# Optimization experiments

Hardware: AMD Instinct MI355X
Metric: run time of the kernel (lower is better)

## Reference

```python
import jax, jax.numpy as jnp
import numpy as np

DIM = 1024
NUM_HEADS = 16
HEAD_DIM = DIM // NUM_HEADS
HIDDEN = 2 * DIM  # swiglu hidden


def rotate_half(x):
    x1, x2 = jnp.split(x, 2, axis=-1)
    return jnp.concatenate((-x2, x1), axis=-1)


def setup_inputs() -> dict:
    key = jax.random.key(0)
    ks = jax.random.split(key, 9)
    s = lambda fan_in: 1.0 / np.sqrt(fan_in)
    x = jax.random.normal(ks[0], (4, 2048, DIM), dtype=jnp.float32)
    qkv_w = jax.random.uniform(ks[1], (3 * DIM, DIM), minval=-s(DIM), maxval=s(DIM))
    proj_w = jax.random.uniform(ks[2], (DIM, DIM), minval=-s(DIM), maxval=s(DIM))
    proj_b = jax.random.uniform(ks[3], (DIM,), minval=-s(DIM), maxval=s(DIM))
    w1_w = jax.random.uniform(ks[4], (HIDDEN, DIM), minval=-s(DIM), maxval=s(DIM))
    w1_b = jnp.zeros((HIDDEN,), jnp.float32)
    w2_w = jax.random.uniform(ks[5], (HIDDEN, DIM), minval=-s(DIM), maxval=s(DIM))
    w2_b = jnp.zeros((HIDDEN,), jnp.float32)
    w3_w = jax.random.uniform(ks[6], (DIM, HIDDEN), minval=-s(HIDDEN), maxval=s(HIDDEN))
    w3_b = jnp.zeros((DIM,), jnp.float32)
    return {"x": x, "qkv_w": qkv_w, "proj_w": proj_w, "proj_b": proj_b,
            "w1_w": w1_w, "w1_b": w1_b, "w2_w": w2_w, "w2_b": w2_b,
            "w3_w": w3_w, "w3_b": w3_b}


def reference(x, qkv_w, proj_w, proj_b, w1_w, w1_b, w2_w, w2_b, w3_w, w3_b):
    B, N, C = x.shape
    H, D = NUM_HEADS, HEAD_DIM
    scale = D ** -0.5
    # QKV projection (no bias)
    qkv = jnp.einsum('bnc,fc->bnf', x, qkv_w).reshape(B, N, 3, H, D)
    qkv = jnp.transpose(qkv, (2, 0, 3, 1, 4))  # [3, B, H, N, D]
    q, k, v = qkv[0], qkv[1], qkv[2]
    # Rotary embeddings
    inv_freq = 1.0 / (10000.0 ** (jnp.arange(0, D, 2, dtype=jnp.float32) / D))
    t = jnp.arange(N, dtype=jnp.float32)
    freqs = jnp.einsum('i,j->ij', t, inv_freq)
    emb = jnp.concatenate((freqs, freqs), axis=-1)[None, None]  # [1,1,N,D]
    cos, sin = jnp.cos(emb), jnp.sin(emb)
    q = q * cos + rotate_half(q) * sin
    k = k * cos + rotate_half(k) * sin
    # Attention (non-causal, as in source)
    attn = jnp.einsum('bhnd,bhmd->bhnm', q, k) * scale
    attn = jax.nn.softmax(attn, axis=-1)
    out = jnp.einsum('bhnm,bhmd->bhnd', attn, v)
    out = jnp.transpose(out, (0, 2, 1, 3)).reshape(B, N, C)
    out = jnp.einsum('bnc,fc->bnf', out, proj_w) + proj_b
    # SwiGLU MLP
    x1 = jnp.einsum('bnc,fc->bnf', out, w1_w) + w1_b
    x2 = jnp.einsum('bnc,fc->bnf', out, w2_w) + w2_b
    hidden = jax.nn.silu(x1) * x2
    return jnp.einsum('bnh,fh->bnf', hidden, w3_w) + w3_b
```

## Files before the change

kernel.cpp:

```cpp
#include <hip/hip_runtime.h>
#include <hip/hip_bf16.h>
#include <math.h>


#define SEQ     2048
#define BATCH   4
#define NH      16
#define CDIM    1024
#define MROWS   8192

typedef __bf16 bf16x8 __attribute__((ext_vector_type(8)));
typedef float  floatx4 __attribute__((ext_vector_type(4)));
typedef float  floatx16 __attribute__((ext_vector_type(16)));
typedef unsigned int u32;

__device__ __forceinline__ unsigned short f2bf(float f) {
    __bf16 h = (__bf16)f;
    return __builtin_bit_cast(unsigned short, h);
}
__device__ __forceinline__ float fexp2(float x) {
    float r; asm("v_exp_f32 %0, %1" : "=v"(r) : "v"(x)); return r;
}
__device__ __forceinline__ floatx4 mfma16(bf16x8 a, bf16x8 b, floatx4 c) {
    return __builtin_amdgcn_mfma_f32_16x16x32_bf16(a, b, c, 0, 0, 0);
}
__device__ __forceinline__ floatx16 mfma32(bf16x8 a, bf16x8 b, floatx16 c) {
    return __builtin_amdgcn_mfma_f32_32x32x16_bf16(a, b, c, 0, 0, 0);
}
__device__ __forceinline__ void gld16(void* lds, const void* g) {
    __builtin_amdgcn_global_load_lds(
        (const __attribute__((address_space(1))) u32*)g,
        (__attribute__((address_space(3))) u32*)lds, 16, 0, 0);
}

template <int OUTMODE, bool BIAS>
__global__ __launch_bounds__(256) void mgemm(
    const unsigned short* __restrict__ A,
    const unsigned short* __restrict__ B,
    const float* __restrict__ bias,
    void* __restrict__ C, int ldc,
    int K)
{
    __shared__ __align__(16) unsigned short As[128 * 32];
    __shared__ __align__(16) unsigned short Bs[128 * 32];

    const int tid  = threadIdx.x;
    const int lane = tid & 63;
    const int wave = tid >> 6;
    const int l16  = lane & 15;
    const int quad = lane >> 4;
    const int wm = (wave >> 1) * 64, wn = (wave & 1) * 64;
    const int bm = blockIdx.y, bn = blockIdx.x;

    const unsigned short* Ag = A + (size_t)(bm * 128) * K;
    const unsigned short* Bg = B + (size_t)(bn * 128) * K;

    const int srow0 = wave * 32 + (lane >> 2);
    const int scol  = (lane & 3) * 8;
    unsigned short* lA0 = As + (wave * 2 + 0) * 512;
    unsigned short* lA1 = As + (wave * 2 + 1) * 512;
    unsigned short* lB0 = Bs + (wave * 2 + 0) * 512;
    unsigned short* lB1 = Bs + (wave * 2 + 1) * 512;
    const unsigned short* gA0 = Ag + (size_t)srow0 * K + scol;
    const unsigned short* gA1 = Ag + (size_t)(srow0 + 16) * K + scol;
    const unsigned short* gB0 = Bg + (size_t)srow0 * K + scol;
    const unsigned short* gB1 = Bg + (size_t)(srow0 + 16) * K + scol;

    floatx4 acc[4][4] = {};

    for (int kt = 0; kt < K; kt += 32) {
        __syncthreads();
        gld16(lA0, gA0 + kt);
        gld16(lA1, gA1 + kt);
        gld16(lB0, gB0 + kt);
        gld16(lB1, gB1 + kt);
        __syncthreads();

        bf16x8 af[4], bfr[4];
        #pragma unroll
        for (int mt = 0; mt < 4; ++mt)
            af[mt] = *(const bf16x8*)&As[(wm + mt * 16 + l16) * 32 + quad * 8];
        #pragma unroll
        for (int nt = 0; nt < 4; ++nt)
            bfr[nt] = *(const bf16x8*)&Bs[(wn + nt * 16 + l16) * 32 + quad * 8];
        #pragma unroll
        for (int mt = 0; mt < 4; ++mt)
            #pragma unroll
            for (int nt = 0; nt < 4; ++nt)
                acc[mt][nt] = mfma16(af[mt], bfr[nt], acc[mt][nt]);
    }

    #pragma unroll
    for (int nt = 0; nt < 4; ++nt) {
        const int gcol = bn * 128 + wn + nt * 16 + l16;
        const float bv = BIAS ? bias[gcol] : 0.0f;
        #pragma unroll
        for (int mt = 0; mt < 4; ++mt) {
            #pragma unroll
            for (int r = 0; r < 4; ++r) {
                const int grow = bm * 128 + wm + mt * 16 + quad * 4 + r;
                float v = acc[mt][nt][r] + bv;
                if (OUTMODE == 0)
                    ((float*)C)[(size_t)grow * ldc + gcol] = v;
                else
                    ((unsigned short*)C)[(size_t)grow * ldc + gcol] = f2bf(v);
            }
        }
    }
}

__global__ __launch_bounds__(256) void mgemm_glu(
    const unsigned short* __restrict__ A,
    const unsigned short* __restrict__ B1,
    const unsigned short* __restrict__ B2,
    const float* __restrict__ bias1,
    const float* __restrict__ bias2,
    unsigned short* __restrict__ C, int ldc,
    int K)
{
    __shared__ __align__(16) unsigned short As[128 * 32];
    __shared__ __align__(16) unsigned short B1s[64 * 32];
    __shared__ __align__(16) unsigned short B2s[64 * 32];

    const int tid  = threadIdx.x;
    const int lane = tid & 63;
    const int wave = tid >> 6;
    const int l16  = lane & 15;
    const int quad = lane >> 4;
    const int wm = (wave >> 1) * 64, wn = (wave & 1) * 32;
    const int bm = blockIdx.y, bn = blockIdx.x;

    const unsigned short* Ag  = A  + (size_t)(bm * 128) * K;
    const unsigned short* B1g = B1 + (size_t)(bn * 64) * K;
    const unsigned short* B2g = B2 + (size_t)(bn * 64) * K;

    const int arow = wave * 32 + (lane >> 2);
    const int brow = wave * 16 + (lane >> 2);
    const int scol = (lane & 3) * 8;
    unsigned short* lA0  = As  + (wave * 2 + 0) * 512;
    unsigned short* lA1  = As  + (wave * 2 + 1) * 512;
    unsigned short* lB1w = B1s + wave * 512;
    unsigned short* lB2w = B2s + wave * 512;
    const unsigned short* gA0 = Ag  + (size_t)arow * K + scol;
    const unsigned short* gA1 = Ag  + (size_t)(arow + 16) * K + scol;
    const unsigned short* gB1 = B1g + (size_t)brow * K + scol;
    const unsigned short* gB2 = B2g + (size_t)brow * K + scol;

    floatx4 acc1[4][2] = {};
    floatx4 acc2[4][2] = {};

    for (int kt = 0; kt < K; kt += 32) {
        __syncthreads();
        gld16(lA0,  gA0 + kt);
        gld16(lA1,  gA1 + kt);
        gld16(lB1w, gB1 + kt);
        gld16(lB2w, gB2 + kt);
        __syncthreads();

        bf16x8 af[4], b1f[2], b2f[2];
        #pragma unroll
        for (int mt = 0; mt < 4; ++mt)
            af[mt] = *(const bf16x8*)&As[(wm + mt * 16 + l16) * 32 + quad * 8];
        #pragma unroll
        for (int nt = 0; nt < 2; ++nt) {
            b1f[nt] = *(const bf16x8*)&B1s[(wn + nt * 16 + l16) * 32 + quad * 8];
            b2f[nt] = *(const bf16x8*)&B2s[(wn + nt * 16 + l16) * 32 + quad * 8];
        }
        #pragma unroll
        for (int mt = 0; mt < 4; ++mt)
            #pragma unroll
            for (int nt = 0; nt < 2; ++nt) {
                acc1[mt][nt] = mfma16(af[mt], b1f[nt], acc1[mt][nt]);
                acc2[mt][nt] = mfma16(af[mt], b2f[nt], acc2[mt][nt]);
            }
    }

    #pragma unroll
    for (int nt = 0; nt < 2; ++nt) {
        const int gcol = bn * 64 + wn + nt * 16 + l16;
        const float b1 = bias1[gcol];
        const float b2 = bias2[gcol];
        #pragma unroll
        for (int mt = 0; mt < 4; ++mt) {
            #pragma unroll
            for (int r = 0; r < 4; ++r) {
                const int grow = bm * 128 + wm + mt * 16 + quad * 4 + r;
                const float x1 = acc1[mt][nt][r] + b1;
                const float x2 = acc2[mt][nt][r] + b2;
                const float v = (x1 / (1.0f + expf(-x1))) * x2;
                C[(size_t)grow * ldc + gcol] = f2bf(v);
            }
        }
    }
}

__global__ __launch_bounds__(256) void mgemm_qkv(
    const unsigned short* __restrict__ A,
    const unsigned short* __restrict__ B,
    const float* __restrict__ tab,
    unsigned short* __restrict__ Qb,
    unsigned short* __restrict__ Kb,
    unsigned short* __restrict__ Vtb)
{
    __shared__ __align__(16) unsigned short As[128 * 32];
    __shared__ __align__(16) unsigned short Bs[128 * 32];

    const int tid  = threadIdx.x;
    const int lane = tid & 63;
    const int wave = tid >> 6;
    const int l16  = lane & 15;
    const int quad = lane >> 4;
    const int wm = (wave >> 1) * 64, wn = (wave & 1) * 64;
    const int bm = blockIdx.y, bn = blockIdx.x;
    const int K = CDIM;

    const unsigned short* Ag = A + (size_t)(bm * 128) * K;
    const unsigned short* Bg = B + (size_t)(bn * 128) * K;

    const int srow0 = wave * 32 + (lane >> 2);
    const int scol  = (lane & 3) * 8;
    unsigned short* lA0 = As + (wave * 2 + 0) * 512;
    unsigned short* lA1 = As + (wave * 2 + 1) * 512;
    unsigned short* lB0 = Bs + (wave * 2 + 0) * 512;
    unsigned short* lB1 = Bs + (wave * 2 + 1) * 512;
    const unsigned short* gA0 = Ag + (size_t)srow0 * K + scol;
    const unsigned short* gA1 = Ag + (size_t)(srow0 + 16) * K + scol;
    const unsigned short* gB0 = Bg + (size_t)srow0 * K + scol;
    const unsigned short* gB1 = Bg + (size_t)(srow0 + 16) * K + scol;

    floatx4 acc[4][4] = {};

    for (int kt = 0; kt < K; kt += 32) {
        __syncthreads();
        gld16(lA0, gA0 + kt);
        gld16(lA1, gA1 + kt);
        gld16(lB0, gB0 + kt);
        gld16(lB1, gB1 + kt);
        __syncthreads();

        bf16x8 af[4], bfr[4];
        #pragma unroll
        for (int mt = 0; mt < 4; ++mt)
            af[mt] = *(const bf16x8*)&As[(wm + mt * 16 + l16) * 32 + quad * 8];
        #pragma unroll
        for (int nt = 0; nt < 4; ++nt)
            bfr[nt] = *(const bf16x8*)&Bs[(wn + nt * 16 + l16) * 32 + quad * 8];
        #pragma unroll
        for (int mt = 0; mt < 4; ++mt)
            #pragma unroll
            for (int nt = 0; nt < 4; ++nt)
                acc[mt][nt] = mfma16(af[mt], bfr[nt], acc[mt][nt]);
    }

    const int colbase0 = bn * 128;
    const int part = colbase0 >> 10;

    if (part == 2) {
        unsigned short* T = As;
        #pragma unroll
        for (int mt = 0; mt < 4; ++mt) {
            __syncthreads();
            #pragma unroll
            for (int nt = 0; nt < 4; ++nt) {
                ushort4 pk;
                pk.x = f2bf(acc[mt][nt][0]); pk.y = f2bf(acc[mt][nt][1]);
                pk.z = f2bf(acc[mt][nt][2]); pk.w = f2bf(acc[mt][nt][3]);
                *(ushort4*)&T[((wave * 64 + nt * 16 + l16) * 16) + quad * 4] = pk;
            }
            __syncthreads();
            const int w2 = tid >> 6, d = tid & 63;
            const int nrow0 = bm * 128 + (w2 >> 1) * 64 + mt * 16;
            const int b = nrow0 >> 11, n0 = nrow0 & 2047;
            const int h2 = ((bn * 128 + (w2 & 1) * 64) & 1023) >> 6;
            unsigned short* dst = Vtb +
                ((size_t)(b * NH + h2) * 64 + d) * 2048 + n0;
            const int tb = (w2 * 64 + d) * 16;
            *(uint4*)dst       = *(const uint4*)&T[tb];
            *(uint4*)(dst + 8) = *(const uint4*)&T[tb + 8];
        }
    } else {
        const float qscale = (part == 0) ? 0.125f * 1.44269504088896f : 1.0f;
        const int h = ((colbase0 + wn) & 1023) >> 6;
        #pragma unroll
        for (int mt = 0; mt < 4; ++mt) {
            #pragma unroll
            for (int r = 0; r < 4; ++r) {
                const int grow = bm * 128 + wm + mt * 16 + quad * 4 + r;
                const int b = grow >> 11, n = grow & 2047;
                unsigned short* dst =
                    (part == 0 ? Qb : Kb) + ((size_t)(b * NH + h) * 2048 + n) * 64;
                #pragma unroll
                for (int nt = 0; nt < 2; ++nt) {
                    const int i = nt * 16 + l16;
                    const float c  = tab[(n * 32 + i) * 2];
                    const float sn = tab[(n * 32 + i) * 2 + 1];
                    const float x1 = acc[mt][nt][r];
                    const float x2v = acc[mt][nt + 2][r];
                    dst[i]      = f2bf((x1 * c - x2v * sn) * qscale);
                    dst[i + 32] = f2bf((x2v * c + x1 * sn) * qscale);
                }
            }
        }
    }
}

__global__ __launch_bounds__(256) void attn_mfma(
    const unsigned short* __restrict__ Qb,
    const unsigned short* __restrict__ Kb,
    const unsigned short* __restrict__ Vtb,
    unsigned short* __restrict__ Ob)
{
    const int qt = blockIdx.x;
    const int bh = blockIdx.y;
    const int tid = threadIdx.x;
    const int lane = tid & 63, wave = tid >> 6;
    const int r32 = lane & 31, hi = lane >> 5;
    const int q0 = wave * 32;
    const int qrow = q0 + r32;

    __shared__ unsigned short QP[128][72];
    __shared__ unsigned short Ks[64][72];
    __shared__ unsigned short Vs[64][72];

    const unsigned short* Qg = Qb + ((size_t)bh * 2048 + qt * 128) * 64;
    const unsigned short* Kg = Kb + (size_t)bh * 2048 * 64;
    const unsigned short* Vg = Vtb + (size_t)bh * 64 * 2048;

    #pragma unroll
    for (int rep = 0; rep < 4; ++rep) {
        const int c = tid + rep * 256;
        const int r = c >> 3, d0 = (c & 7) * 8;
        *(uint4*)&QP[r][d0] = *(const uint4*)(Qg + (size_t)r * 64 + d0);
    }

    const int c0 = tid, c1 = tid + 256;
    const int kr0 = c0 >> 3, kd0 = (c0 & 7) * 8;
    const int kr1 = c1 >> 3, kd1 = (c1 & 7) * 8;

    uint4 ka0 = *(const uint4*)(Kg + (size_t)kr0 * 64 + kd0);
    uint4 ka1 = *(const uint4*)(Kg + (size_t)kr1 * 64 + kd1);
    uint4 va0 = *(const uint4*)(Vg + (size_t)kr0 * 2048 + kd0);
    uint4 va1 = *(const uint4*)(Vg + (size_t)kr1 * 2048 + kd1);

    __syncthreads();

    bf16x8 bq[4];
    #pragma unroll
    for (int f = 0; f < 4; ++f)
        bq[f] = *(const bf16x8*)&QP[qrow][f * 16 + hi * 8];

    floatx16 o0 = {}, o1 = {};
    float l_acc = 0.0f;

    for (int kt = 0; kt < 32; ++kt) {
        __syncthreads();
        *(uint4*)&Ks[kr0][kd0] = ka0;
        *(uint4*)&Ks[kr1][kd1] = ka1;
        *(uint4*)&Vs[kr0][kd0] = va0;
        *(uint4*)&Vs[kr1][kd1] = va1;
        if (kt + 1 < 32) {
            const size_t nb = (size_t)(kt + 1) * 64;
            ka0 = *(const uint4*)(Kg + (nb + kr0) * 64 + kd0);
            ka1 = *(const uint4*)(Kg + (nb + kr1) * 64 + kd1);
            va0 = *(const uint4*)(Vg + (size_t)kr0 * 2048 + nb + kd0);
            va1 = *(const uint4*)(Vg + (size_t)kr1 * 2048 + nb + kd1);
        }
        __syncthreads();

        #pragma unroll
        for (int t = 0; t < 2; ++t) {
            floatx16 s = {};
            #pragma unroll
            for (int f = 0; f < 4; ++f) {
                const bf16x8 ak = *(const bf16x8*)&Ks[t * 32 + r32][f * 16 + hi * 8];
                s = mfma32(ak, bq[f], s);
            }
            float rs = 0.0f;
            #pragma unroll
            for (int g = 0; g < 4; ++g) {
                const float p0 = fexp2(s[4 * g + 0]);
                const float p1 = fexp2(s[4 * g + 1]);
                const float p2 = fexp2(s[4 * g + 2]);
                const float p3 = fexp2(s[4 * g + 3]);
                rs += (p0 + p1) + (p2 + p3);
                ushort4 pk;
                pk.x = f2bf(p0); pk.y = f2bf(p1); pk.z = f2bf(p2); pk.w = f2bf(p3);
                *(ushort4*)&QP[qrow][t * 32 + 8 * g + 4 * hi] = pk;
            }
            l_acc += rs;
        }

        bf16x8 bp[4];
        #pragma unroll
        for (int f = 0; f < 4; ++f)
            bp[f] = *(const bf16x8*)&QP[qrow][f * 16 + hi * 8];
        #pragma unroll
        for (int f = 0; f < 4; ++f) {
            const bf16x8 av0 = *(const bf16x8*)&Vs[r32][f * 16 + hi * 8];
            o0 = mfma32(av0, bp[f], o0);
            const bf16x8 av1 = *(const bf16x8*)&Vs[32 + r32][f * 16 + hi * 8];
            o1 = mfma32(av1, bp[f], o1);
        }
    }

    const float l_tot = l_acc + __shfl_xor(l_acc, 32);
    const float inv = 1.0f / l_tot;
    const int b = bh >> 4, h = bh & 15;
    unsigned short* orow = Ob +
        (size_t)(b * SEQ + qt * 128 + qrow) * CDIM + h * 64;
    #pragma unroll
    for (int u = 0; u < 2; ++u) {
        const floatx16 ov = u ? o1 : o0;
        #pragma unroll
        for (int g = 0; g < 4; ++g) {
            ushort4 pk;
            pk.x = f2bf(ov[4 * g + 0] * inv); pk.y = f2bf(ov[4 * g + 1] * inv);
            pk.z = f2bf(ov[4 * g + 2] * inv); pk.w = f2bf(ov[4 * g + 3] * inv);
            *(ushort4*)(orow + u * 32 + 8 * g + 4 * hi) = pk;
        }
    }
}

__global__ __launch_bounds__(256) void cvt_bf16(
    const float* __restrict__ src, unsigned short* __restrict__ dst)
{
    const size_t i = ((size_t)blockIdx.x * 256 + threadIdx.x) * 4;
    const float4 f = *(const float4*)(src + i);
    ushort4 o; o.x = f2bf(f.x); o.y = f2bf(f.y); o.z = f2bf(f.z); o.w = f2bf(f.w);
    *(ushort4*)(dst + i) = o;
}

__global__ __launch_bounds__(256) void rope_table(float* __restrict__ tab)
{
    const int idx = blockIdx.x * 256 + threadIdx.x;
    const int i = idx & 31, n = idx >> 5;
    const double f = (double)n * pow(10000.0, -(double)(2 * i) / 64.0);
    tab[idx * 2]     = (float)cos(f);
    tab[idx * 2 + 1] = (float)sin(f);
}

extern "C" void kernel_launch(void* const* d_in, const int* in_sizes, int n_in,
                              void* d_out, int out_size, void* d_ws, size_t ws_size,
                              hipStream_t stream)
{
    const float* x      = (const float*)d_in[0];
    const float* qkv_w  = (const float*)d_in[1];
    const float* proj_w = (const float*)d_in[2];
    const float* proj_b = (const float*)d_in[3];
    const float* w1_w   = (const float*)d_in[4];
    const float* w1_b   = (const float*)d_in[5];
    const float* w2_w   = (const float*)d_in[6];
    const float* w2_b   = (const float*)d_in[7];
    const float* w3_w   = (const float*)d_in[8];
    const float* w3_b   = (const float*)d_in[9];
    float* out = (float*)d_out;

    char* ws = (char*)d_ws;
    unsigned short* Qb    = (unsigned short*)(ws);
    unsigned short* Kb    = (unsigned short*)(ws + 16777216);
    unsigned short* Vtb   = (unsigned short*)(ws + 33554432);
    unsigned short* Ob    = (unsigned short*)(ws + 50331648);
    unsigned short* out1b = (unsigned short*)(ws + 67108864);
    unsigned short* w1b   = (unsigned short*)(ws + 83886080);
    unsigned short* w2b   = (unsigned short*)(ws + 88080384);
    unsigned short* w3b   = (unsigned short*)(ws + 92274688);
    unsigned short* projb = (unsigned short*)(ws + 96468992);
    unsigned short* xb    = (unsigned short*)(ws + 98566144);
    unsigned short* wqkvb = (unsigned short*)(ws + 115343360);
    float*          tab   = (float*)(ws + 121634816);
    unsigned short* hid   = (unsigned short*)(ws);

    const dim3 blk(256);

    cvt_bf16<<<dim3(8192), blk, 0, stream>>>(x, xb);
    cvt_bf16<<<dim3(3072), blk, 0, stream>>>(qkv_w, wqkvb);
    cvt_bf16<<<dim3(1024), blk, 0, stream>>>(proj_w, projb);
    cvt_bf16<<<dim3(2048), blk, 0, stream>>>(w1_w, w1b);
    cvt_bf16<<<dim3(2048), blk, 0, stream>>>(w2_w, w2b);
    cvt_bf16<<<dim3(2048), blk, 0, stream>>>(w3_w, w3b);
    rope_table<<<dim3(256), blk, 0, stream>>>(tab);

    mgemm_qkv<<<dim3(24, 64), blk, 0, stream>>>(xb, wqkvb, tab, Qb, Kb, Vtb);
    attn_mfma<<<dim3(SEQ / 128, BATCH * NH), blk, 0, stream>>>(Qb, Kb, Vtb, Ob);
    mgemm<1, true><<<dim3(8, 64), blk, 0, stream>>>(
        Ob, projb, proj_b, out1b, CDIM, CDIM);
    mgemm_glu<<<dim3(32, 64), blk, 0, stream>>>(
        out1b, w1b, w2b, w1_b, w2_b, hid, 2048, CDIM);
    mgemm<0, true><<<dim3(8, 64), blk, 0, stream>>>(
        hid, w3b, w3_b, out, CDIM, 2048);
}
```

Before: 503.6 us.

## Keep softmax probabilities in registers via permlane swap, merge conversions, reorder attention grid

The attention kernel no longer writes the exponentiated scores to LDS and reads them back. Instead it packs them to bf16 with v_cvt_pk_bf16_f32 and rearranges lanes with v_permlane32_swap so they can feed the PV MFMA directly. The six separate fp32-to-bf16 conversion launches are merged into one kernel that picks its source and destination by index range. The attention grid axes are also swapped so consecutive blocks walk across heads rather than query tiles. Together these remove LDS round trips and launch overhead, but they depend on the lane permutation exactly matching the MFMA operand layout.

```diff
diff --git a/kernel.cpp b/kernel.cpp
--- a/kernel.cpp
+++ b/kernel.cpp
@@ -20,6 +20,10 @@
 }
 __device__ __forceinline__ float fexp2(float x) {
     float r; asm("v_exp_f32 %0, %1" : "=v"(r) : "v"(x)); return r;
+}
+__device__ __forceinline__ u32 cvtpk(float lo, float hi) {
+    u32 w; asm("v_cvt_pk_bf16_f32 %0, %1, %2" : "=v"(w) : "v"(lo), "v"(hi));
+    return w;
 }
 __device__ __forceinline__ floatx4 mfma16(bf16x8 a, bf16x8 b, floatx4 c) {
     return __builtin_amdgcn_mfma_f32_16x16x32_bf16(a, b, c, 0, 0, 0);
@@ -310,13 +314,12 @@
     const unsigned short* __restrict__ Vtb,
     unsigned short* __restrict__ Ob)
 {
-    const int qt = blockIdx.x;
-    const int bh = blockIdx.y;
+    const int bh = blockIdx.x;
+    const int qt = blockIdx.y;
     const int tid = threadIdx.x;
     const int lane = tid & 63, wave = tid >> 6;
     const int r32 = lane & 31, hi = lane >> 5;
-    const int q0 = wave * 32;
-    const int qrow = q0 + r32;
+    const int qrow = wave * 32 + r32;
 
     __shared__ unsigned short QP[128][72];
     __shared__ unsigned short Ks[64][72];
@@ -375,31 +378,34 @@
                 const bf16x8 ak = *(const bf16x8*)&Ks[t * 32 + r32][f * 16 + hi * 8];
                 s = mfma32(ak, bq[f], s);
             }
+            float p[16];
             float rs = 0.0f;
             #pragma unroll
-            for (int g = 0; g < 4; ++g) {
-                const float p0 = fexp2(s[4 * g + 0]);
-                const float p1 = fexp2(s[4 * g + 1]);
-                const float p2 = fexp2(s[4 * g + 2]);
-                const float p3 = fexp2(s[4 * g + 3]);
-                rs += (p0 + p1) + (p2 + p3);
-                ushort4 pk;
-                pk.x = f2bf(p0); pk.y = f2bf(p1); pk.z = f2bf(p2); pk.w = f2bf(p3);
-                *(ushort4*)&QP[qrow][t * 32 + 8 * g + 4 * hi] = pk;
-            }
+            for (int g = 0; g < 16; ++g) { p[g] = fexp2(s[g]); rs += p[g]; }
             l_acc += rs;
-        }
-
-        bf16x8 bp[4];
-        #pragma unroll
-        for (int f = 0; f < 4; ++f)
-            bp[f] = *(const bf16x8*)&QP[qrow][f * 16 + hi * 8];
-        #pragma unroll
-        for (int f = 0; f < 4; ++f) {
-            const bf16x8 av0 = *(const bf16x8*)&Vs[r32][f * 16 + hi * 8];
-            o0 = mfma32(av0, bp[f], o0);
-            const bf16x8 av1 = *(const bf16x8*)&Vs[32 + r32][f * 16 + hi * 8];
-            o1 = mfma32(av1, bp[f], o1);
+            u32 w0 = cvtpk(p[0], p[1]),   w2 = cvtpk(p[4], p[5]);
+            u32 w1 = cvtpk(p[2], p[3]),   w3 = cvtpk(p[6], p[7]);
+            u32 w4 = cvtpk(p[8], p[9]),   w6 = cvtpk(p[12], p[13]);
+            u32 w5 = cvtpk(p[10], p[11]), w7 = cvtpk(p[14], p[15]);
+            asm("v_permlane32_swap_b32 %0, %1" : "+v"(w0), "+v"(w2));
+            asm("v_permlane32_swap_b32 %0, %1" : "+v"(w1), "+v"(w3));
+            asm("v_permlane32_swap_b32 %0, %1" : "+v"(w4), "+v"(w6));
+            asm("v_permlane32_swap_b32 %0, %1" : "+v"(w5), "+v"(w7));
+            uint4 u0; u0.x = w0; u0.y = w1; u0.z = w2; u0.w = w3;
+            uint4 u1; u1.x = w4; u1.y = w5; u1.z = w6; u1.w = w7;
+            const bf16x8 bp0 = __builtin_bit_cast(bf16x8, u0);
+            const bf16x8 bp1 = __builtin_bit_cast(bf16x8, u1);
+            {
+                const int f0 = 2 * t, f1 = 2 * t + 1;
+                const bf16x8 av00 = *(const bf16x8*)&Vs[r32][f0 * 16 + hi * 8];
+                const bf16x8 av01 = *(const bf16x8*)&Vs[32 + r32][f0 * 16 + hi * 8];
+                o0 = mfma32(av00, bp0, o0);
+                o1 = mfma32(av01, bp0, o1);
+                const bf16x8 av10 = *(const bf16x8*)&Vs[r32][f1 * 16 + hi * 8];
+                const bf16x8 av11 = *(const bf16x8*)&Vs[32 + r32][f1 * 16 + hi * 8];
+                o0 = mfma32(av10, bp1, o0);
+                o1 = mfma32(av11, bp1, o1);
+            }
         }
     }
 
@@ -421,13 +427,26 @@
     }
 }
 
-__global__ __launch_bounds__(256) void cvt_bf16(
-    const float* __restrict__ src, unsigned short* __restrict__ dst)
+__global__ __launch_bounds__(256) void cvt_all(
+    const float* __restrict__ x,    const float* __restrict__ qkv,
+    const float* __restrict__ proj, const float* __restrict__ w1,
+    const float* __restrict__ w2,   const float* __restrict__ w3,
+    unsigned short* __restrict__ xb,    unsigned short* __restrict__ qkvb,
+    unsigned short* __restrict__ projb, unsigned short* __restrict__ w1b,
+    unsigned short* __restrict__ w2b,   unsigned short* __restrict__ w3b)
 {
     const size_t i = ((size_t)blockIdx.x * 256 + threadIdx.x) * 4;
-    const float4 f = *(const float4*)(src + i);
+    const float* src; unsigned short* dst; size_t off;
+    if      (i <  8388608) { src = x;    dst = xb;    off = 0; }
+    else if (i < 11534336) { src = qkv;  dst = qkvb;  off = 8388608; }
+    else if (i < 12582912) { src = proj; dst = projb; off = 11534336; }
+    else if (i < 14680064) { src = w1;   dst = w1b;   off = 12582912; }
+    else if (i < 16777216) { src = w2;   dst = w2b;   off = 14680064; }
+    else                   { src = w3;   dst = w3b;   off = 16777216; }
+    const size_t j = i - off;
+    const float4 f = *(const float4*)(src + j);
     ushort4 o; o.x = f2bf(f.x); o.y = f2bf(f.y); o.z = f2bf(f.z); o.w = f2bf(f.w);
-    *(ushort4*)(dst + i) = o;
+    *(ushort4*)(dst + j) = o;
 }
 
 __global__ __launch_bounds__(256) void rope_table(float* __restrict__ tab)
@@ -472,16 +491,13 @@
 
     const dim3 blk(256);
 
-    cvt_bf16<<<dim3(8192), blk, 0, stream>>>(x, xb);
-    cvt_bf16<<<dim3(3072), blk, 0, stream>>>(qkv_w, wqkvb);
-    cvt_bf16<<<dim3(1024), blk, 0, stream>>>(proj_w, projb);
-    cvt_bf16<<<dim3(2048), blk, 0, stream>>>(w1_w, w1b);
-    cvt_bf16<<<dim3(2048), blk, 0, stream>>>(w2_w, w2b);
-    cvt_bf16<<<dim3(2048), blk, 0, stream>>>(w3_w, w3b);
+    cvt_all<<<dim3(18432), blk, 0, stream>>>(
+        x, qkv_w, proj_w, w1_w, w2_w, w3_w,
+        xb, wqkvb, projb, w1b, w2b, w3b);
     rope_table<<<dim3(256), blk, 0, stream>>>(tab);
 
     mgemm_qkv<<<dim3(24, 64), blk, 0, stream>>>(xb, wqkvb, tab, Qb, Kb, Vtb);
-    attn_mfma<<<dim3(SEQ / 128, BATCH * NH), blk, 0, stream>>>(Qb, Kb, Vtb, Ob);
+    attn_mfma<<<dim3(BATCH * NH, SEQ / 128), blk, 0, stream>>>(Qb, Kb, Vtb, Ob);
     mgemm<1, true><<<dim3(8, 64), blk, 0, stream>>>(
         Ob, projb, proj_b, out1b, CDIM, CDIM);
     mgemm_glu<<<dim3(32, 64), blk, 0, stream>>>(
```

Result: faster. 492.0 us (-2.3%).
